# Kernel optimization log

Measured on AMD Instinct MI355X. Metric: run time of the kernel, lower is better.

## Reference

```python
import jax, jax.numpy as jnp
import numpy as np

V_THRESH = 0.3

@jax.custom_vjp
def spike(x):
    return (x > 0).astype(x.dtype)

def _spike_fwd(x):
    return spike(x), x

def _spike_bwd(x, g):
    # rectangular straight-through surrogate gradient (pass grad where |x| < 0.5)
    return (g * (jnp.abs(x) < 0.5).astype(g.dtype),)

spike.defvjp(_spike_fwd, _spike_bwd)


def setup_inputs() -> dict:
    key = jax.random.key(0)
    B, T, H = 128, 2048, 128
    k1, = jax.random.split(key, 1)
    x_seq = jax.random.normal(k1, (B, T, H), dtype=jnp.float32)
    v0 = jnp.zeros((B, H), dtype=jnp.float32)
    z0 = jnp.zeros((B, H), dtype=jnp.float32)
    decay_raw = jnp.zeros((H,), dtype=jnp.float32)  # nn.initializers.constant(0.0)
    return {"x_seq": x_seq, "v0": v0, "z0": z0, "decay_raw": decay_raw}


def reference(x_seq, v0, z0, decay_raw):
    # LIF recurrence: v_t = v_{t-1} * decay * (1 - z_{t-1}) + x_t ; z_t = spike(v_t - v_thresh)
    decay = jax.nn.sigmoid(decay_raw)  # (H,)

    def step(carry, x_t):
        v, z = carry
        v = v * decay * (1.0 - z) + x_t
        z_out = spike(v - V_THRESH)
        return (v, z_out), z_out

    x_tb = jnp.swapaxes(x_seq, 0, 1)  # [T, B, H] for lax.scan over time
    (_, _), spk_tb = jax.lax.scan(step, (v0, z0), x_tb)
    return jnp.swapaxes(spk_tb, 0, 1)  # [B, T, H]
```

## Files before the change

### kernel.cpp

```cpp
#include <hip/hip_runtime.h>
#include <math.h>


constexpr int Bdim = 128;
constexpr int Tdim = 2048;
constexpr int Hdim = 128;
constexpr int HW   = 64;
constexpr int U    = 128;
constexpr int NBUF = 4;
constexpr int NW   = 8;
constexpr int NTILE = Tdim / U;
constexpr float VTH = 0.3f;

typedef const __attribute__((address_space(1))) void* gptr_t;
typedef __attribute__((address_space(3))) void* lptr_t;

__global__ __launch_bounds__(NW * 64) void lif_kernel(
    const float* __restrict__ x,
    const float* __restrict__ v0,
    const float* __restrict__ z0,
    const float* __restrict__ decay_raw,
    float* __restrict__ out)
{
    __shared__ float lds[NBUF][U][HW];

    const int tid  = threadIdx.x;
    const int wave = tid >> 6;
    const int lane = tid & 63;
    const int blk  = blockIdx.x;
    const int b    = blk >> 1;
    const int h0   = (blk & 1) * HW;

    const float* xbase = x   + (size_t)b * Tdim * Hdim + h0;
    float*       obase = out + (size_t)b * Tdim * Hdim + h0;

    const int sub = (lane >> 4) * Hdim + (lane & 15) * 4;

    auto fill = [&](int tile, int buf) {
        const float* g = xbase + (size_t)tile * U * Hdim + sub;
        #pragma unroll
        for (int q = 0; q < 4; ++q) {
            const int jj = wave * 4 + q;
            __builtin_amdgcn_global_load_lds(
                (gptr_t)(const void*)(g + (size_t)(4 * jj) * Hdim),
                (lptr_t)(void*)&lds[buf][4 * jj][0],
                16, 0, 0);
        }
    };

    auto flush = [&](int tile, int buf) {
        #pragma unroll
        for (int q = 0; q < 4; ++q) {
            const int s   = wave * 4 + q;
            const int row = 4 * s + (lane >> 4);
            const int col = (lane & 15) * 4;
            const float4 vv = *(const float4*)&lds[buf][row][col];
            *(float4*)(obase + (size_t)(tile * U + row) * Hdim + col) = vv;
        }
    };

    float decay = 0.f, v = 0.f, z = 0.f;
    if (wave == 0) {
        decay = 1.0f / (1.0f + expf(-decay_raw[h0 + lane]));
        v = v0[b * Hdim + h0 + lane];
        z = z0[b * Hdim + h0 + lane];
    }

    fill(0, 0);
    fill(1, 1);
    __syncthreads();

    for (int k = 0; k < NTILE; ++k) {
        if (k + 2 < NTILE) fill(k + 2, (k + 2) % NBUF);
        if (k >= 1)        flush(k - 1, (k - 1) % NBUF);

        if (wave == 0) {
            const int cb = k % NBUF;
            #pragma unroll 16
            for (int tl = 0; tl < U; ++tl) {
                const float xv = lds[cb][tl][lane];
                const float vd = v * decay;
                v = ((z > 0.5f) ? 0.0f : vd) + xv;
                z = (v > VTH) ? 1.0f : 0.0f;
                lds[cb][tl][lane] = z;
            }
        }
        __syncthreads();
    }
    flush(NTILE - 1, (NTILE - 1) % NBUF);
}

extern "C" void kernel_launch(void* const* d_in, const int* in_sizes, int n_in,
                              void* d_out, int out_size, void* d_ws, size_t ws_size,
                              hipStream_t stream) {
    const float* x         = (const float*)d_in[0];
    const float* v0        = (const float*)d_in[1];
    const float* z0        = (const float*)d_in[2];
    const float* decay_raw = (const float*)d_in[3];
    float* out = (float*)d_out;

    lif_kernel<<<Bdim * Hdim / HW, NW * 64, 0, stream>>>(x, v0, z0, decay_raw, out);
}
```

Before: 240.8 us.

## Warp-specialize LIF kernel with producer/compute/consumer waves and LDS flag sync

Replaces the block-wide __syncthreads tile loop with warp specialization. Two loader waves alternate filling a 5-deep x ring, one wave runs the recurrence into a separate 3-deep z ring, and one wave stores results, all coordinated through volatile LDS flags with spin-sleeps. The goal is to keep the serial recurrence wave from stalling at barriers and to overlap loads and stores continuously. It also cuts the block to 4 waves and halves the tile size. It relies on the ordering of the flag protocol and on s_waitcnt counts, which is a correctness risk.

Result: slower. 246.6 us (+2.4%).

```diff
diff --git a/kernel.cpp b/kernel.cpp
--- a/kernel.cpp
+++ b/kernel.cpp
@@ -6,23 +6,30 @@
 constexpr int Tdim = 2048;
 constexpr int Hdim = 128;
 constexpr int HW   = 64;
-constexpr int U    = 128;
-constexpr int NBUF = 4;
-constexpr int NW   = 8;
-constexpr int NTILE = Tdim / U;
+constexpr int Ut   = 64;
+constexpr int NT   = Tdim / Ut;
+constexpr int NX   = 5;
+constexpr int NZ   = 3;
 constexpr float VTH = 0.3f;
+
 
 typedef const __attribute__((address_space(1))) void* gptr_t;
 typedef __attribute__((address_space(3))) void* lptr_t;
 
-__global__ __launch_bounds__(NW * 64) void lif_kernel(
+__device__ __forceinline__ void cfence() { asm volatile("" ::: "memory"); }
+
+__global__ __launch_bounds__(256) void lif_kernel(
     const float* __restrict__ x,
     const float* __restrict__ v0,
     const float* __restrict__ z0,
     const float* __restrict__ decay_raw,
     float* __restrict__ out)
 {
-    __shared__ float lds[NBUF][U][HW];
+    __shared__ float xbuf[NX][Ut][HW];
+    __shared__ float zbuf[NZ][Ut][HW];
+    __shared__ int   flags[8];
+
+    volatile int* vf = (volatile int*)flags;
 
     const int tid  = threadIdx.x;
     const int wave = tid >> 6;
@@ -31,63 +38,74 @@
     const int b    = blk >> 1;
     const int h0   = (blk & 1) * HW;
 
+    if (tid < 8) flags[tid] = 0;
+    __syncthreads();
+
     const float* xbase = x   + (size_t)b * Tdim * Hdim + h0;
     float*       obase = out + (size_t)b * Tdim * Hdim + h0;
-
     const int sub = (lane >> 4) * Hdim + (lane & 15) * 4;
 
-    auto fill = [&](int tile, int buf) {
-        const float* g = xbase + (size_t)tile * U * Hdim + sub;
-        #pragma unroll
-        for (int q = 0; q < 4; ++q) {
-            const int jj = wave * 4 + q;
-            __builtin_amdgcn_global_load_lds(
-                (gptr_t)(const void*)(g + (size_t)(4 * jj) * Hdim),
-                (lptr_t)(void*)&lds[buf][4 * jj][0],
-                16, 0, 0);
+    if (wave == 1 || wave == 3) {
+        const int par = (wave == 1) ? 0 : 1;
+        for (int i = 0; i < NT / 2; ++i) {
+            const int k = 2 * i + par;
+            while (vf[2] < k - NX + 1) __builtin_amdgcn_s_sleep(2);
+            cfence();
+            const float* g = xbase + (size_t)k * Ut * Hdim + sub;
+            float* lbase = &xbuf[k % NX][0][0];
+            #pragma unroll
+            for (int j = 0; j < Ut / 4; ++j) {
+                __builtin_amdgcn_global_load_lds(
+                    (gptr_t)(const void*)(g + (size_t)(4 * j) * Hdim),
+                    (lptr_t)(void*)(lbase + 4 * j * HW),
+                    16, 0, 0);
+            }
+            asm volatile("s_waitcnt vmcnt(16)" ::: "memory");
+            if (lane == 0) vf[par] = i;
         }
-    };
+        asm volatile("s_waitcnt vmcnt(0)" ::: "memory");
+        if (lane == 0) vf[par] = NT / 2;
+    } else if (wave == 0) {
+        const float decay = 1.0f / (1.0f + expf(-decay_raw[h0 + lane]));
+        float v = v0[b * Hdim + h0 + lane];
+        float z = z0[b * Hdim + h0 + lane];
 
-    auto flush = [&](int tile, int buf) {
-        #pragma unroll
-        for (int q = 0; q < 4; ++q) {
-            const int s   = wave * 4 + q;
-            const int row = 4 * s + (lane >> 4);
-            const int col = (lane & 15) * 4;
-            const float4 vv = *(const float4*)&lds[buf][row][col];
-            *(float4*)(obase + (size_t)(tile * U + row) * Hdim + col) = vv;
+        for (int k = 0; k < NT; ++k) {
+            const int need = (k >> 1) + 1;
+            while (vf[k & 1] < need) __builtin_amdgcn_s_sleep(2);
+            while (vf[4] < k - NZ + 1) __builtin_amdgcn_s_sleep(2);
+            cfence();
+            const int xb = k % NX, zb = k % NZ;
+            #pragma unroll 16
+            for (int t = 0; t < Ut; ++t) {
+                const float xv = xbuf[xb][t][lane];
+                const float a  = v * decay + 0.0f;
+                const float s  = a + xv;
+                v = (z > 0.5f) ? xv : s;
+                z = (v > VTH) ? 1.0f : 0.0f;
+                zbuf[zb][t][lane] = z;
+            }
+            asm volatile("s_waitcnt lgkmcnt(0)" ::: "memory");
+            if (lane == 0) { vf[3] = k + 1; vf[2] = k + 1; }
         }
-    };
-
-    float decay = 0.f, v = 0.f, z = 0.f;
-    if (wave == 0) {
-        decay = 1.0f / (1.0f + expf(-decay_raw[h0 + lane]));
-        v = v0[b * Hdim + h0 + lane];
-        z = z0[b * Hdim + h0 + lane];
+    } else {
+        for (int k = 0; k < NT; ++k) {
+            while (vf[3] < k + 1) __builtin_amdgcn_s_sleep(2);
+            cfence();
+            const int zb = k % NZ;
+            float* op = obase + (size_t)k * Ut * Hdim;
+            #pragma unroll
+            for (int s = 0; s < Ut / 4; ++s) {
+                const int row = 4 * s + (lane >> 4);
+                const int col = (lane & 15) * 4;
+                const float4 vv = *(const float4*)&zbuf[zb][row][col];
+                *(float4*)(op + (size_t)row * Hdim + col) = vv;
+            }
+            cfence();
+            if (lane == 0) vf[4] = k + 1;
+            asm volatile("s_waitcnt vmcnt(16)" ::: "memory");
+        }
     }
-
-    fill(0, 0);
-    fill(1, 1);
-    __syncthreads();
-
-    for (int k = 0; k < NTILE; ++k) {
-        if (k + 2 < NTILE) fill(k + 2, (k + 2) % NBUF);
-        if (k >= 1)        flush(k - 1, (k - 1) % NBUF);
-
-        if (wave == 0) {
-            const int cb = k % NBUF;
-            #pragma unroll 16
-            for (int tl = 0; tl < U; ++tl) {
-                const float xv = lds[cb][tl][lane];
-                const float vd = v * decay;
-                v = ((z > 0.5f) ? 0.0f : vd) + xv;
-                z = (v > VTH) ? 1.0f : 0.0f;
-                lds[cb][tl][lane] = z;
-            }
-        }
-        __syncthreads();
-    }
-    flush(NTILE - 1, (NTILE - 1) % NBUF);
 }
 
 extern "C" void kernel_launch(void* const* d_in, const int* in_sizes, int n_in,
@@ -99,5 +117,5 @@
     const float* decay_raw = (const float*)d_in[3];
     float* out = (float*)d_out;
 
-    lif_kernel<<<Bdim * Hdim / HW, NW * 64, 0, stream>>>(x, v0, z0, decay_raw, out);
+    lif_kernel<<<Bdim * Hdim / HW, 256, 0, stream>>>(x, v0, z0, decay_raw, out);
 }
```
